# Kernel tuning notes

Measured on AMD Instinct MI355X. Metric: run time of the kernel, lower is better.

## Reference

```python
import jax, jax.numpy as jnp
import numpy as np

K = 256      # model / per-head dim (module uses full k per head)
H = 8        # heads
B = 4
T = 2048
EPS = 1e-5   # nn.LayerNorm default eps


def _layernorm(x, gamma, beta):
    mu = jnp.mean(x, axis=-1, keepdims=True)
    var = jnp.mean(jnp.square(x - mu), axis=-1, keepdims=True)
    return (x - mu) * jax.lax.rsqrt(var + EPS) * gamma + beta


def setup_inputs() -> dict:
    key = jax.random.key(0)
    ks = jax.random.split(key, 12)
    s = lambda fan_in: 1.0 / np.sqrt(fan_in)
    return {
        "x":  jax.random.normal(ks[0], (B, T, K), dtype=jnp.float32),
        # attention projections, stored (in, out) for x @ W
        "wq": jax.random.uniform(ks[1], (K, K * H), jnp.float32, -s(K), s(K)),
        "wk": jax.random.uniform(ks[2], (K, K * H), jnp.float32, -s(K), s(K)),
        "wv": jax.random.uniform(ks[3], (K, K * H), jnp.float32, -s(K), s(K)),
        "wu": jax.random.uniform(ks[4], (K * H, K), jnp.float32, -s(K * H), s(K * H)),
        "bu": jnp.zeros((K,), jnp.float32),
        # feed-forward
        "w1": jax.random.uniform(ks[5], (K, 4 * K), jnp.float32, -s(K), s(K)),
        "b1": jnp.zeros((4 * K,), jnp.float32),
        "w2": jax.random.uniform(ks[6], (4 * K, K), jnp.float32, -s(4 * K), s(4 * K)),
        "b2": jnp.zeros((K,), jnp.float32),
        # layernorms
        "g1": jnp.ones((K,), jnp.float32),
        "be1": jnp.zeros((K,), jnp.float32),
        "g2": jnp.ones((K,), jnp.float32),
        "be2": jnp.zeros((K,), jnp.float32),
    }


def reference(x, wq, wk, wv, wu, bu, w1, b1, w2, b2, g1, be1, g2, be2):
    b, t, k = x.shape
    h = H
    scale = k ** (-0.25)  # applied to both q and k, as in the torch code
    q = (x @ wq).reshape(b, t, h, k).transpose(0, 2, 1, 3) * scale  # bhtk
    kk = (x @ wk).reshape(b, t, h, k).transpose(0, 2, 1, 3) * scale
    v = (x @ wv).reshape(b, t, h, k).transpose(0, 2, 1, 3)
    dot = jnp.einsum("bhtk,bhsk->bhts", q, kk)
    # masked=True: upper triangle (offset=1) set to -inf -> causal
    causal = jnp.tril(jnp.ones((t, t), dtype=bool))
    dot = jnp.where(causal, dot, -jnp.inf)
    attn = jax.nn.softmax(dot, axis=-1)
    out = jnp.einsum("bhts,bhsk->bhtk", attn, v)
    out = out.transpose(0, 2, 1, 3).reshape(b, t, h * k)
    attn_out = out @ wu + bu

    x = x + attn_out                    # residual=True
    x = _layernorm(x, g1, be1)          # norm=True
    ff = jnp.maximum(x @ w1 + b1, 0.0) @ w2 + b2
    x = x + ff                          # ff + residual
    x = _layernorm(x, g2, be2)
    return x
```

## Files before the change

kernel.cpp:

```cpp
#include <hip/hip_runtime.h>
#include <hip/hip_bf16.h>

#define TT 2048
#define BB 4
#define HH 8
#define KK 256
#define MM (BB*TT)
#define NQKV 6144
#define QKS 4096

typedef __attribute__((ext_vector_type(8))) short bf16x8;
typedef __attribute__((ext_vector_type(4))) float f32x4;

__device__ __forceinline__ void gld_lds16(const void* g, void* lds) {
    __builtin_amdgcn_global_load_lds(
        (const __attribute__((address_space(1))) unsigned int*)g,
        (__attribute__((address_space(3))) unsigned int*)lds, 16, 0, 0);
}

__global__ __launch_bounds__(256) void cvt_k(const float* __restrict__ in,
                                             __hip_bfloat16* __restrict__ out, int n) {
    int i = (blockIdx.x * 256 + threadIdx.x) * 4;
    if (i + 3 < n) {
        float4 v = *(const float4*)(in + i);
        out[i + 0] = __float2bfloat16(v.x);
        out[i + 1] = __float2bfloat16(v.y);
        out[i + 2] = __float2bfloat16(v.z);
        out[i + 3] = __float2bfloat16(v.w);
    }
}

__global__ __launch_bounds__(256) void transpose_cvt(const float* __restrict__ in,
                                                     __hip_bfloat16* __restrict__ out,
                                                     int R, int C) {
    __shared__ float tile[32][33];
    int c0 = blockIdx.x * 32, r0 = blockIdx.y * 32;
    int tx = threadIdx.x & 31, ty = threadIdx.x >> 5;
    #pragma unroll
    for (int i = ty; i < 32; i += 8)
        tile[i][tx] = in[(size_t)(r0 + i) * C + c0 + tx];
    __syncthreads();
    #pragma unroll
    for (int i = ty; i < 32; i += 8)
        out[(size_t)(c0 + i) * R + r0 + tx] = __float2bfloat16(tile[tx][i]);
}

template<int EPI, int BN>
__global__ __launch_bounds__(256) void gemm_k(const __hip_bfloat16* __restrict__ A,
                                              const __hip_bfloat16* __restrict__ Bt,
                                              int M, int N, int Kd,
                                              const float* __restrict__ bias,
                                              const float* __restrict__ res,
                                              void* __restrict__ outp, float scale,
                                              __hip_bfloat16* __restrict__ vtp) {
    __shared__ short sA[2][128 * 32];
    __shared__ short sB[2][BN * 32];
    int tid = threadIdx.x, lane = tid & 63, wave = tid >> 6;
    int l15 = lane & 15, g = lane >> 4;
    int m0 = blockIdx.y * 128, n0 = blockIdx.x * BN;
    constexpr int NF = BN / 32;
    int wm = (wave >> 1) * 64, wn = (wave & 1) * (BN / 2);
    f32x4 acc[4][NF] = {};
    const int NT = Kd >> 5;

    int arow0 = tid >> 2, acol = (tid & 3) * 8;
    int arow1 = (tid + 256) >> 2;

    auto STAGE = [&](int kt, int buf) {
        size_t ka = (size_t)kt * 32 + acol;
        gld_lds16(A + (size_t)(m0 + arow0) * Kd + ka, (char*)sA[buf] + wave * 1024);
        gld_lds16(A + (size_t)(m0 + arow1) * Kd + ka, (char*)sA[buf] + 4096 + wave * 1024);
        gld_lds16(Bt + (size_t)(n0 + arow0) * Kd + ka, (char*)sB[buf] + wave * 1024);
        if (BN == 128)
            gld_lds16(Bt + (size_t)(n0 + arow1) * Kd + ka, (char*)sB[buf] + 4096 + wave * 1024);
    };

    STAGE(0, 0);
    asm volatile("s_waitcnt vmcnt(0)" ::: "memory");
    __syncthreads();
    int cur = 0;
    for (int kt = 0; kt < NT; ++kt) {
        if (kt + 1 < NT) STAGE(kt + 1, cur ^ 1);
        bf16x8 af[4], bfr[NF];
        #pragma unroll
        for (int mf = 0; mf < 4; ++mf)
            af[mf] = *(const bf16x8*)&sA[cur][(wm + mf * 16 + l15) * 32 + g * 8];
        #pragma unroll
        for (int nf = 0; nf < NF; ++nf)
            bfr[nf] = *(const bf16x8*)&sB[cur][(wn + nf * 16 + l15) * 32 + g * 8];
        #pragma unroll
        for (int mf = 0; mf < 4; ++mf)
            #pragma unroll
            for (int nf = 0; nf < NF; ++nf)
                acc[mf][nf] = __builtin_amdgcn_mfma_f32_16x16x32_bf16(af[mf], bfr[nf], acc[mf][nf], 0, 0, 0);
        asm volatile("s_waitcnt vmcnt(0)" ::: "memory");
        __syncthreads();
        cur ^= 1;
    }

    #pragma unroll
    for (int mf = 0; mf < 4; ++mf) {
        int rowb = m0 + wm + mf * 16 + g * 4;
        #pragma unroll
        for (int nf = 0; nf < NF; ++nf) {
            int col = n0 + wn + nf * 16 + l15;
            if (EPI == 0) {
                if (col < 4096) {
                    #pragma unroll
                    for (int r = 0; r < 4; ++r)
                        ((__hip_bfloat16*)outp)[(size_t)(rowb + r) * QKS + col] =
                            __float2bfloat16(acc[mf][nf][r] * scale);
                } else {
                    int hv = col - 4096, h = hv >> 8, d = hv & 255;
                    int b = rowb >> 11, t = rowb & 2047;
                    ushort4 w;
                    w.x = __bfloat16_as_ushort(__float2bfloat16(acc[mf][nf][0]));
                    w.y = __bfloat16_as_ushort(__float2bfloat16(acc[mf][nf][1]));
                    w.z = __bfloat16_as_ushort(__float2bfloat16(acc[mf][nf][2]));
                    w.w = __bfloat16_as_ushort(__float2bfloat16(acc[mf][nf][3]));
                    *(ushort4*)(vtp + ((size_t)((b * 8 + h) * 256 + d)) * TT + t) = w;
                }
            } else {
                #pragma unroll
                for (int r = 0; r < 4; ++r) {
                    float v = acc[mf][nf][r];
                    size_t idx = (size_t)(rowb + r) * N + col;
                    if (EPI == 1) {
                        ((float*)outp)[idx] = v + bias[col] + res[idx];
                    } else {
                        v += bias[col];
                        ((__hip_bfloat16*)outp)[idx] = __float2bfloat16(v > 0.0f ? v : 0.0f);
                    }
                }
            }
        }
    }
}

__global__ __launch_bounds__(512, 2) void attn_k(const __hip_bfloat16* __restrict__ QK,
                                                 const __hip_bfloat16* __restrict__ VT,
                                                 __hip_bfloat16* __restrict__ O) {
    __shared__ char Kl[2][32768];
    __shared__ char Vl[2][32768];
    __shared__ char Pl[8][2048];
    int tid = threadIdx.x, lane = tid & 63, wave = tid >> 6;
    int id = blockIdx.x;
    int xcd = id & 7, w = id >> 3;
    int bh = xcd * 4 + (w >> 3);
    int jtp = w & 7;
    int b = bh >> 3, h = bh & 7;
    const __hip_bfloat16* Qb = QK + (size_t)b * TT * QKS + h * KK;
    const __hip_bfloat16* Kb = Qb + 2048;
    const __hip_bfloat16* Vtb = VT + (size_t)bh * KK * TT;

    int l15 = lane & 15, g = lane >> 4;
    int koff = g * 8;
    int koffB = g * 16;
    int pswz = (l15 & 7) << 4;

    auto STAGE = [&](int s0, int buf) {
        #pragma unroll
        for (int rd = 0; rd < 4; ++rd) {
            int L = rd * 8192 + tid * 16;
            int row = L >> 9;
            int cb = (L & 511) ^ ((row & 7) << 4);
            gld_lds16((const char*)(Kb + (size_t)(s0 + row) * QKS) + cb,
                      Kl[buf] + rd * 8192 + wave * 1024);
        }
        #pragma unroll
        for (int rd = 0; rd < 4; ++rd) {
            int L = rd * 8192 + tid * 16;
            int row = L >> 7;
            int cb = (L & 127) ^ ((row & 7) << 4);
            gld_lds16((const char*)(Vtb + (size_t)row * TT + s0) + cb,
                      Vl[buf] + rd * 8192 + wave * 1024);
        }
    };

    #pragma unroll 1
    for (int half = 0; half < 2; ++half) {
        int jt = (half == 0) ? jtp : 15 - jtp;
        int q0 = jt * 128;
        int rowbase = q0 + wave * 16;
        bf16x8 qf[8];
        #pragma unroll
        for (int kk = 0; kk < 8; ++kk)
            qf[kk] = *(const bf16x8*)(Qb + (size_t)(rowbase + l15) * QKS + kk * 32 + koff);

        f32x4 Oa[16] = {};
        float mrow = -__builtin_inff();
        float lrow = 0.f;

        STAGE(0, 0);
        asm volatile("s_waitcnt vmcnt(0)" ::: "memory");
        __syncthreads();
        int cur = 0;
        const int niter = 2 * jt + 2;

        #pragma unroll 1
        for (int i = 0; i < niter; ++i) {
            int s0 = i * 64;
            if (i + 1 < niter) STAGE(s0 + 64, cur ^ 1);

            if (s0 <= rowbase + 15) {
                f32x4 S[4] = {};
                __builtin_amdgcn_s_setprio(1);
                #pragma unroll
                for (int nf = 0; nf < 4; ++nf) {
                    int r = nf * 16 + l15;
                    int swz = (r & 7) << 4;
                    #pragma unroll
                    for (int kk = 0; kk < 8; ++kk) {
                        bf16x8 kf = *(const bf16x8*)(Kl[cur] + r * 512 + ((kk * 64 + koffB) ^ swz));
                        S[nf] = __builtin_amdgcn_mfma_f32_16x16x32_bf16(kf, qf[kk], S[nf], 0, 0, 0);
                    }
                }
                __builtin_amdgcn_s_setprio(0);
                if (s0 + 63 > rowbase) {
                    int qg = rowbase + l15;
                    #pragma unroll
                    for (int nf = 0; nf < 4; ++nf)
                        #pragma unroll
                        for (int r = 0; r < 4; ++r) {
                            int sg = s0 + nf * 16 + g * 4 + r;
                            if (sg > qg) S[nf][r] = -__builtin_inff();
                        }
                }
                float mx = S[0][0];
                #pragma unroll
                for (int nf = 0; nf < 4; ++nf)
                    #pragma unroll
                    for (int r = 0; r < 4; ++r) mx = fmaxf(mx, S[nf][r]);
                mx = fmaxf(mx, __shfl_xor(mx, 16));
                mx = fmaxf(mx, __shfl_xor(mx, 32));
                if (__any(mx > mrow + 8.0f)) {
                    float mn = fmaxf(mrow, mx);
                    float alpha = exp2f(mrow - mn);
                    mrow = mn;
                    lrow *= alpha;
                    float al[4];
                    #pragma unroll
                    for (int r = 0; r < 4; ++r) al[r] = __shfl(alpha, (g << 2) + r);
                    #pragma unroll
                    for (int nf2 = 0; nf2 < 16; ++nf2)
                        #pragma unroll
                        for (int r = 0; r < 4; ++r) Oa[nf2][r] *= al[r];
                }
                float ps = 0.f;
                #pragma unroll
                for (int nf = 0; nf < 4; ++nf)
                    #pragma unroll
                    for (int r = 0; r < 4; ++r) {
                        float p = exp2f(S[nf][r] - mrow);
                        S[nf][r] = p; ps += p;
                    }
                ps += __shfl_xor(ps, 16);
                ps += __shfl_xor(ps, 32);
                lrow += ps;
                #pragma unroll
                for (int nf = 0; nf < 4; ++nf) {
                    uint2 pk2;
                    pk2.x = (unsigned)__bfloat16_as_ushort(__float2bfloat16(S[nf][0]))
                          | ((unsigned)__bfloat16_as_ushort(__float2bfloat16(S[nf][1])) << 16);
                    pk2.y = (unsigned)__bfloat16_as_ushort(__float2bfloat16(S[nf][2]))
                          | ((unsigned)__bfloat16_as_ushort(__float2bfloat16(S[nf][3])) << 16);
                    *(uint2*)(Pl[wave] + l15 * 128 + ((nf * 32 + g * 8) ^ pswz)) = pk2;
                }
                bf16x8 pa[2];
                #pragma unroll
                for (int kk2 = 0; kk2 < 2; ++kk2)
                    pa[kk2] = *(const bf16x8*)(Pl[wave] + l15 * 128 + ((kk2 * 64 + koffB) ^ pswz));
                __builtin_amdgcn_s_setprio(1);
                #pragma unroll
                for (int nf2 = 0; nf2 < 16; ++nf2) {
                    int r = nf2 * 16 + l15;
                    int swz = (r & 7) << 4;
                    #pragma unroll
                    for (int kk2 = 0; kk2 < 2; ++kk2) {
                        bf16x8 vb = *(const bf16x8*)(Vl[cur] + r * 128 + ((kk2 * 64 + koffB) ^ swz));
                        Oa[nf2] = __builtin_amdgcn_mfma_f32_16x16x32_bf16(pa[kk2], vb, Oa[nf2], 0, 0, 0);
                    }
                }
                __builtin_amdgcn_s_setprio(0);
            }
            asm volatile("s_waitcnt vmcnt(0)" ::: "memory");
            __syncthreads();
            cur ^= 1;
        }
        float rcp_ = 1.0f / lrow;
        float rc[4];
        #pragma unroll
        for (int r = 0; r < 4; ++r) rc[r] = __shfl(rcp_, (g << 2) + r);
        #pragma unroll
        for (int nf2 = 0; nf2 < 16; ++nf2) {
            int col = nf2 * 16 + l15;
            #pragma unroll
            for (int r = 0; r < 4; ++r) {
                int t = rowbase + g * 4 + r;
                O[((size_t)b * TT + t) * 2048 + h * KK + col] = __float2bfloat16(Oa[nf2][r] * rc[r]);
            }
        }
    }
}

__global__ __launch_bounds__(256) void layernorm_k(const float* __restrict__ y,
                                                   const float* __restrict__ g,
                                                   const float* __restrict__ be,
                                                   float* __restrict__ out_f,
                                                   __hip_bfloat16* __restrict__ out_b) {
    int row = blockIdx.x * 4 + (threadIdx.x >> 6);
    int lane = threadIdx.x & 63;
    float4 v = *(const float4*)(y + (size_t)row * 256 + lane * 4);
    float s = v.x + v.y + v.z + v.w;
    #pragma unroll
    for (int d = 1; d < 64; d <<= 1) s += __shfl_xor(s, d);
    float mu = s * (1.0f / 256.0f);
    float dx = v.x - mu, dy = v.y - mu, dz = v.z - mu, dw = v.w - mu;
    float q = dx * dx + dy * dy + dz * dz + dw * dw;
    #pragma unroll
    for (int d = 1; d < 64; d <<= 1) q += __shfl_xor(q, d);
    float rs = rsqrtf(q * (1.0f / 256.0f) + 1e-5f);
    float4 gg = *(const float4*)(g + lane * 4);
    float4 bb = *(const float4*)(be + lane * 4);
    float4 o;
    o.x = dx * rs * gg.x + bb.x;
    o.y = dy * rs * gg.y + bb.y;
    o.z = dz * rs * gg.z + bb.z;
    o.w = dw * rs * gg.w + bb.w;
    *(float4*)(out_f + (size_t)row * 256 + lane * 4) = o;
    if (out_b) {
        size_t i = (size_t)row * 256 + lane * 4;
        out_b[i + 0] = __float2bfloat16(o.x);
        out_b[i + 1] = __float2bfloat16(o.y);
        out_b[i + 2] = __float2bfloat16(o.z);
        out_b[i + 3] = __float2bfloat16(o.w);
    }
}

extern "C" void kernel_launch(void* const* d_in, const int* in_sizes, int n_in,
                              void* d_out, int out_size, void* d_ws, size_t ws_size,
                              hipStream_t stream) {
    const float* x  = (const float*)d_in[0];
    const float* wq = (const float*)d_in[1];
    const float* wk = (const float*)d_in[2];
    const float* wv = (const float*)d_in[3];
    const float* wu = (const float*)d_in[4];
    const float* bu = (const float*)d_in[5];
    const float* w1 = (const float*)d_in[6];
    const float* b1 = (const float*)d_in[7];
    const float* w2 = (const float*)d_in[8];
    const float* b2 = (const float*)d_in[9];
    const float* g1 = (const float*)d_in[10];
    const float* be1 = (const float*)d_in[11];
    const float* g2 = (const float*)d_in[12];
    const float* be2 = (const float*)d_in[13];

    char* p = (char*)d_ws;
    auto alloc = [&](size_t bytes) { char* r = p; p += bytes; return r; };
    __hip_bfloat16* xb    = (__hip_bfloat16*)alloc((size_t)MM * KK * 2);
    __hip_bfloat16* wqkvT = (__hip_bfloat16*)alloc((size_t)NQKV * KK * 2);
    __hip_bfloat16* wuT   = (__hip_bfloat16*)alloc((size_t)KK * 2048 * 2);
    __hip_bfloat16* w1T   = (__hip_bfloat16*)alloc((size_t)1024 * KK * 2);
    __hip_bfloat16* w2T   = (__hip_bfloat16*)alloc((size_t)KK * 1024 * 2);
    __hip_bfloat16* qk    = (__hip_bfloat16*)alloc((size_t)MM * QKS * 2);
    __hip_bfloat16* vt    = (__hip_bfloat16*)alloc((size_t)32 * KK * TT * 2);
    __hip_bfloat16* attn  = (__hip_bfloat16*)alloc((size_t)MM * 2048 * 2);
    float*          y1    = (float*)alloc((size_t)MM * KK * 4);
    float*          x1    = (float*)alloc((size_t)MM * KK * 4);
    __hip_bfloat16* x1b   = (__hip_bfloat16*)alloc((size_t)MM * KK * 2);
    __hip_bfloat16* hid   = (__hip_bfloat16*)alloc((size_t)MM * 1024 * 2);
    float*          y2    = (float*)alloc((size_t)MM * KK * 4);

    cvt_k<<<(MM * KK) / 1024, 256, 0, stream>>>(x, xb, MM * KK);
    transpose_cvt<<<dim3(64, 8),  256, 0, stream>>>(wq, wqkvT,             256, 2048);
    transpose_cvt<<<dim3(64, 8),  256, 0, stream>>>(wk, wqkvT + 2048 * 256, 256, 2048);
    transpose_cvt<<<dim3(64, 8),  256, 0, stream>>>(wv, wqkvT + 4096 * 256, 256, 2048);
    transpose_cvt<<<dim3(8, 64),  256, 0, stream>>>(wu, wuT, 2048, 256);
    transpose_cvt<<<dim3(32, 8),  256, 0, stream>>>(w1, w1T, 256, 1024);
    transpose_cvt<<<dim3(8, 32),  256, 0, stream>>>(w2, w2T, 1024, 256);

    gemm_k<0, 128><<<dim3(NQKV / 128, MM / 128), 256, 0, stream>>>(
        xb, wqkvT, MM, NQKV, 256, nullptr, nullptr, qk, 0.3002806f, vt);

    attn_k<<<dim3(256), 512, 0, stream>>>(qk, vt, attn);

    gemm_k<1, 64><<<dim3(4, MM / 128), 256, 0, stream>>>(
        attn, wuT, MM, 256, 2048, bu, x, y1, 1.0f, nullptr);
    layernorm_k<<<MM / 4, 256, 0, stream>>>(y1, g1, be1, x1, x1b);

    gemm_k<2, 128><<<dim3(8, MM / 128), 256, 0, stream>>>(
        x1b, w1T, MM, 1024, 256, b1, nullptr, hid, 1.0f, nullptr);
    gemm_k<1, 64><<<dim3(4, MM / 128), 256, 0, stream>>>(
        hid, w2T, MM, 256, 1024, b2, x1, y2, 1.0f, nullptr);
    layernorm_k<<<MM / 4, 256, 0, stream>>>(y2, g2, be2, (float*)d_out, nullptr);
}
```

Baseline: 260.3 us.

## Restructure attention to 4-wave blocks with 32 query rows per wave, single-buffered

The attention kernel moves from 512-thread blocks that each process two causal tiles to 512 blocks of 256 threads, each handling one query tile. Each wave now owns 32 query rows, so every K and V fragment read from LDS feeds two MFMAs. K/V staging drops double buffering, so loads are no longer overlapped with compute, in exchange for half the LDS per block. Separately, the GEMM LDS tiles gain an XOR swizzle on the A/B rows to reduce bank conflicts.

```diff
diff --git a/kernel.cpp b/kernel.cpp
--- a/kernel.cpp
+++ b/kernel.cpp
@@ -63,11 +63,12 @@
     f32x4 acc[4][NF] = {};
     const int NT = Kd >> 5;
 
-    int arow0 = tid >> 2, acol = (tid & 3) * 8;
-    int arow1 = (tid + 256) >> 2;
+    int arow0 = tid >> 2;
+    int arow1 = arow0 + 64;
+    int sl = ((tid & 3) ^ ((arow0 >> 1) & 3)) * 8;
 
     auto STAGE = [&](int kt, int buf) {
-        size_t ka = (size_t)kt * 32 + acol;
+        size_t ka = (size_t)kt * 32 + sl;
         gld_lds16(A + (size_t)(m0 + arow0) * Kd + ka, (char*)sA[buf] + wave * 1024);
         gld_lds16(A + (size_t)(m0 + arow1) * Kd + ka, (char*)sA[buf] + 4096 + wave * 1024);
         gld_lds16(Bt + (size_t)(n0 + arow0) * Kd + ka, (char*)sB[buf] + wave * 1024);
@@ -83,11 +84,15 @@
         if (kt + 1 < NT) STAGE(kt + 1, cur ^ 1);
         bf16x8 af[4], bfr[NF];
         #pragma unroll
-        for (int mf = 0; mf < 4; ++mf)
-            af[mf] = *(const bf16x8*)&sA[cur][(wm + mf * 16 + l15) * 32 + g * 8];
-        #pragma unroll
-        for (int nf = 0; nf < NF; ++nf)
-            bfr[nf] = *(const bf16x8*)&sB[cur][(wn + nf * 16 + l15) * 32 + g * 8];
+        for (int mf = 0; mf < 4; ++mf) {
+            int row = wm + mf * 16 + l15;
+            af[mf] = *(const bf16x8*)((char*)sA[cur] + row * 64 + ((g ^ ((row >> 1) & 3)) * 16));
+        }
+        #pragma unroll
+        for (int nf = 0; nf < NF; ++nf) {
+            int row = wn + nf * 16 + l15;
+            bfr[nf] = *(const bf16x8*)((char*)sB[cur] + row * 64 + ((g ^ ((row >> 1) & 3)) * 16));
+        }
         #pragma unroll
         for (int mf = 0; mf < 4; ++mf)
             #pragma unroll
@@ -137,17 +142,18 @@
     }
 }
 
-__global__ __launch_bounds__(512, 2) void attn_k(const __hip_bfloat16* __restrict__ QK,
+__global__ __launch_bounds__(256, 2) void attn_k(const __hip_bfloat16* __restrict__ QK,
                                                  const __hip_bfloat16* __restrict__ VT,
                                                  __hip_bfloat16* __restrict__ O) {
-    __shared__ char Kl[2][32768];
-    __shared__ char Vl[2][32768];
-    __shared__ char Pl[8][2048];
+    __shared__ char Kl[32768];
+    __shared__ char Vl[32768];
+    __shared__ char Pl[4][4096];
     int tid = threadIdx.x, lane = tid & 63, wave = tid >> 6;
     int id = blockIdx.x;
     int xcd = id & 7, w = id >> 3;
-    int bh = xcd * 4 + (w >> 3);
-    int jtp = w & 7;
+    int half = w >> 5, w5 = w & 31;
+    int bh = xcd * 4 + (w5 & 3);
+    int jt = half ? (w5 >> 2) : 15 - (w5 >> 2);
     int b = bh >> 3, h = bh & 7;
     const __hip_bfloat16* Qb = QK + (size_t)b * TT * QKS + h * KK;
     const __hip_bfloat16* Kb = Qb + 2048;
@@ -158,136 +164,142 @@
     int koffB = g * 16;
     int pswz = (l15 & 7) << 4;
 
-    auto STAGE = [&](int s0, int buf) {
-        #pragma unroll
-        for (int rd = 0; rd < 4; ++rd) {
-            int L = rd * 8192 + tid * 16;
+    auto STAGE = [&](int s0) {
+        #pragma unroll
+        for (int rd = 0; rd < 8; ++rd) {
+            int L = rd * 4096 + tid * 16;
             int row = L >> 9;
             int cb = (L & 511) ^ ((row & 7) << 4);
             gld_lds16((const char*)(Kb + (size_t)(s0 + row) * QKS) + cb,
-                      Kl[buf] + rd * 8192 + wave * 1024);
-        }
-        #pragma unroll
-        for (int rd = 0; rd < 4; ++rd) {
-            int L = rd * 8192 + tid * 16;
+                      Kl + rd * 4096 + wave * 1024);
+        }
+        #pragma unroll
+        for (int rd = 0; rd < 8; ++rd) {
+            int L = rd * 4096 + tid * 16;
             int row = L >> 7;
             int cb = (L & 127) ^ ((row & 7) << 4);
             gld_lds16((const char*)(Vtb + (size_t)row * TT + s0) + cb,
-                      Vl[buf] + rd * 8192 + wave * 1024);
+                      Vl + rd * 4096 + wave * 1024);
         }
     };
 
+    int q0 = jt * 128;
+    int rowbase = q0 + wave * 32;
+    bf16x8 qf[2][8];
+    #pragma unroll
+    for (int f = 0; f < 2; ++f)
+        #pragma unroll
+        for (int kk = 0; kk < 8; ++kk)
+            qf[f][kk] = *(const bf16x8*)(Qb + (size_t)(rowbase + f * 16 + l15) * QKS + kk * 32 + koff);
+
+    f32x4 Oa[2][16] = {};
+    float mrow[2] = {-__builtin_inff(), -__builtin_inff()};
+    float lrow[2] = {0.f, 0.f};
+    const int niter = 2 * jt + 2;
+
     #pragma unroll 1
-    for (int half = 0; half < 2; ++half) {
-        int jt = (half == 0) ? jtp : 15 - jtp;
-        int q0 = jt * 128;
-        int rowbase = q0 + wave * 16;
-        bf16x8 qf[8];
-        #pragma unroll
-        for (int kk = 0; kk < 8; ++kk)
-            qf[kk] = *(const bf16x8*)(Qb + (size_t)(rowbase + l15) * QKS + kk * 32 + koff);
-
-        f32x4 Oa[16] = {};
-        float mrow = -__builtin_inff();
-        float lrow = 0.f;
-
-        STAGE(0, 0);
+    for (int i = 0; i < niter; ++i) {
+        int s0 = i * 64;
+        STAGE(s0);
         asm volatile("s_waitcnt vmcnt(0)" ::: "memory");
         __syncthreads();
-        int cur = 0;
-        const int niter = 2 * jt + 2;
-
-        #pragma unroll 1
-        for (int i = 0; i < niter; ++i) {
-            int s0 = i * 64;
-            if (i + 1 < niter) STAGE(s0 + 64, cur ^ 1);
-
-            if (s0 <= rowbase + 15) {
-                f32x4 S[4] = {};
-                __builtin_amdgcn_s_setprio(1);
-                #pragma unroll
-                for (int nf = 0; nf < 4; ++nf) {
-                    int r = nf * 16 + l15;
-                    int swz = (r & 7) << 4;
-                    #pragma unroll
-                    for (int kk = 0; kk < 8; ++kk) {
-                        bf16x8 kf = *(const bf16x8*)(Kl[cur] + r * 512 + ((kk * 64 + koffB) ^ swz));
-                        S[nf] = __builtin_amdgcn_mfma_f32_16x16x32_bf16(kf, qf[kk], S[nf], 0, 0, 0);
-                    }
-                }
-                __builtin_amdgcn_s_setprio(0);
-                if (s0 + 63 > rowbase) {
-                    int qg = rowbase + l15;
+
+        if (s0 <= rowbase + 31) {
+            f32x4 S[2][4] = {{}, {}};
+            __builtin_amdgcn_s_setprio(1);
+            #pragma unroll
+            for (int nf = 0; nf < 4; ++nf) {
+                int r = nf * 16 + l15;
+                int swz = (r & 7) << 4;
+                #pragma unroll
+                for (int kk = 0; kk < 8; ++kk) {
+                    bf16x8 kf = *(const bf16x8*)(Kl + r * 512 + ((kk * 64 + koffB) ^ swz));
+                    S[0][nf] = __builtin_amdgcn_mfma_f32_16x16x32_bf16(kf, qf[0][kk], S[0][nf], 0, 0, 0);
+                    S[1][nf] = __builtin_amdgcn_mfma_f32_16x16x32_bf16(kf, qf[1][kk], S[1][nf], 0, 0, 0);
+                }
+            }
+            __builtin_amdgcn_s_setprio(0);
+            if (s0 + 63 > rowbase) {
+                #pragma unroll
+                for (int f = 0; f < 2; ++f) {
+                    int qg = rowbase + f * 16 + l15;
                     #pragma unroll
                     for (int nf = 0; nf < 4; ++nf)
                         #pragma unroll
                         for (int r = 0; r < 4; ++r) {
                             int sg = s0 + nf * 16 + g * 4 + r;
-                            if (sg > qg) S[nf][r] = -__builtin_inff();
+                            if (sg > qg) S[f][nf][r] = -__builtin_inff();
                         }
                 }
-                float mx = S[0][0];
+            }
+            #pragma unroll
+            for (int f = 0; f < 2; ++f) {
+                float mx = S[f][0][0];
                 #pragma unroll
                 for (int nf = 0; nf < 4; ++nf)
                     #pragma unroll
-                    for (int r = 0; r < 4; ++r) mx = fmaxf(mx, S[nf][r]);
+                    for (int r = 0; r < 4; ++r) mx = fmaxf(mx, S[f][nf][r]);
                 mx = fmaxf(mx, __shfl_xor(mx, 16));
                 mx = fmaxf(mx, __shfl_xor(mx, 32));
-                if (__any(mx > mrow + 8.0f)) {
-                    float mn = fmaxf(mrow, mx);
-                    float alpha = exp2f(mrow - mn);
-                    mrow = mn;
-                    lrow *= alpha;
+                if (__any(mx > mrow[f] + 8.0f)) {
+                    float mn = fmaxf(mrow[f], mx);
+                    float alpha = exp2f(mrow[f] - mn);
+                    mrow[f] = mn;
+                    lrow[f] *= alpha;
                     float al[4];
                     #pragma unroll
                     for (int r = 0; r < 4; ++r) al[r] = __shfl(alpha, (g << 2) + r);
                     #pragma unroll
                     for (int nf2 = 0; nf2 < 16; ++nf2)
                         #pragma unroll
-                        for (int r = 0; r < 4; ++r) Oa[nf2][r] *= al[r];
+                        for (int r = 0; r < 4; ++r) Oa[f][nf2][r] *= al[r];
                 }
                 float ps = 0.f;
                 #pragma unroll
                 for (int nf = 0; nf < 4; ++nf)
                     #pragma unroll
                     for (int r = 0; r < 4; ++r) {
-                        float p = exp2f(S[nf][r] - mrow);
-                        S[nf][r] = p; ps += p;
+                        float p = exp2f(S[f][nf][r] - mrow[f]);
+                        S[f][nf][r] = p; ps += p;
                     }
                 ps += __shfl_xor(ps, 16);
                 ps += __shfl_xor(ps, 32);
-                lrow += ps;
+                lrow[f] += ps;
                 #pragma unroll
                 for (int nf = 0; nf < 4; ++nf) {
                     uint2 pk2;
-                    pk2.x = (unsigned)__bfloat16_as_ushort(__float2bfloat16(S[nf][0]))
-                          | ((unsigned)__bfloat16_as_ushort(__float2bfloat16(S[nf][1])) << 16);
-                    pk2.y = (unsigned)__bfloat16_as_ushort(__float2bfloat16(S[nf][2]))
-                          | ((unsigned)__bfloat16_as_ushort(__float2bfloat16(S[nf][3])) << 16);
-                    *(uint2*)(Pl[wave] + l15 * 128 + ((nf * 32 + g * 8) ^ pswz)) = pk2;
-                }
-                bf16x8 pa[2];
-                #pragma unroll
-                for (int kk2 = 0; kk2 < 2; ++kk2)
-                    pa[kk2] = *(const bf16x8*)(Pl[wave] + l15 * 128 + ((kk2 * 64 + koffB) ^ pswz));
-                __builtin_amdgcn_s_setprio(1);
-                #pragma unroll
-                for (int nf2 = 0; nf2 < 16; ++nf2) {
-                    int r = nf2 * 16 + l15;
-                    int swz = (r & 7) << 4;
-                    #pragma unroll
-                    for (int kk2 = 0; kk2 < 2; ++kk2) {
-                        bf16x8 vb = *(const bf16x8*)(Vl[cur] + r * 128 + ((kk2 * 64 + koffB) ^ swz));
-                        Oa[nf2] = __builtin_amdgcn_mfma_f32_16x16x32_bf16(pa[kk2], vb, Oa[nf2], 0, 0, 0);
-                    }
-                }
-                __builtin_amdgcn_s_setprio(0);
-            }
-            asm volatile("s_waitcnt vmcnt(0)" ::: "memory");
-            __syncthreads();
-            cur ^= 1;
-        }
-        float rcp_ = 1.0f / lrow;
+                    pk2.x = (unsigned)__bfloat16_as_ushort(__float2bfloat16(S[f][nf][0]))
+                          | ((unsigned)__bfloat16_as_ushort(__float2bfloat16(S[f][nf][1])) << 16);
+                    pk2.y = (unsigned)__bfloat16_as_ushort(__float2bfloat16(S[f][nf][2]))
+                          | ((unsigned)__bfloat16_as_ushort(__float2bfloat16(S[f][nf][3])) << 16);
+                    *(uint2*)(Pl[wave] + (f * 16 + l15) * 128 + ((nf * 32 + g * 8) ^ pswz)) = pk2;
+                }
+            }
+            bf16x8 pa0[2], pa1[2];
+            #pragma unroll
+            for (int kk2 = 0; kk2 < 2; ++kk2) {
+                pa0[kk2] = *(const bf16x8*)(Pl[wave] + (l15) * 128 + ((kk2 * 64 + koffB) ^ pswz));
+                pa1[kk2] = *(const bf16x8*)(Pl[wave] + (16 + l15) * 128 + ((kk2 * 64 + koffB) ^ pswz));
+            }
+            __builtin_amdgcn_s_setprio(1);
+            #pragma unroll
+            for (int nf2 = 0; nf2 < 16; ++nf2) {
+                int r = nf2 * 16 + l15;
+                int swz = (r & 7) << 4;
+                #pragma unroll
+                for (int kk2 = 0; kk2 < 2; ++kk2) {
+                    bf16x8 vb = *(const bf16x8*)(Vl + r * 128 + ((kk2 * 64 + koffB) ^ swz));
+                    Oa[0][nf2] = __builtin_amdgcn_mfma_f32_16x16x32_bf16(pa0[kk2], vb, Oa[0][nf2], 0, 0, 0);
+                    Oa[1][nf2] = __builtin_amdgcn_mfma_f32_16x16x32_bf16(pa1[kk2], vb, Oa[1][nf2], 0, 0, 0);
+                }
+            }
+            __builtin_amdgcn_s_setprio(0);
+        }
+        __syncthreads();
+    }
+    #pragma unroll
+    for (int f = 0; f < 2; ++f) {
+        float rcp_ = 1.0f / lrow[f];
         float rc[4];
         #pragma unroll
         for (int r = 0; r < 4; ++r) rc[r] = __shfl(rcp_, (g << 2) + r);
@@ -296,8 +308,8 @@
             int col = nf2 * 16 + l15;
             #pragma unroll
             for (int r = 0; r < 4; ++r) {
-                int t = rowbase + g * 4 + r;
-                O[((size_t)b * TT + t) * 2048 + h * KK + col] = __float2bfloat16(Oa[nf2][r] * rc[r]);
+                int t = rowbase + f * 16 + g * 4 + r;
+                O[((size_t)b * TT + t) * 2048 + h * KK + col] = __float2bfloat16(Oa[f][nf2][r] * rc[r]);
             }
         }
     }
@@ -382,7 +394,7 @@
     gemm_k<0, 128><<<dim3(NQKV / 128, MM / 128), 256, 0, stream>>>(
         xb, wqkvT, MM, NQKV, 256, nullptr, nullptr, qk, 0.3002806f, vt);
 
-    attn_k<<<dim3(256), 512, 0, stream>>>(qk, vt, attn);
+    attn_k<<<dim3(512), 256, 0, stream>>>(qk, vt, attn);
 
     gemm_k<1, 64><<<dim3(4, MM / 128), 256, 0, stream>>>(
         attn, wuT, MM, 256, 2048, bu, x, y1, 1.0f, nullptr);
```

Measured after the change: 411.1 us. 57.9% more time.

## Widen GEMM K-tile to 64 with XOR-swizzled LDS layout

Applied to the files above, without the earlier changes.

The GEMM main loop now stages 64-wide K slices per iteration instead of 32, halving the number of barrier and wait round-trips, and performs two MFMA sub-steps per stage. LDS rows are laid out with an XOR swizzle so the 16-byte fragment reads avoid bank conflicts. This doubles shared memory use per block, which may lower occupancy, and relies on Kd being a multiple of 64.

```diff
diff --git a/kernel.cpp b/kernel.cpp
--- a/kernel.cpp
+++ b/kernel.cpp
@@ -53,26 +53,36 @@
                                               const float* __restrict__ res,
                                               void* __restrict__ outp, float scale,
                                               __hip_bfloat16* __restrict__ vtp) {
-    __shared__ short sA[2][128 * 32];
-    __shared__ short sB[2][BN * 32];
+    constexpr int NF = BN / 32;
+    constexpr int BPHYS = BN / 4;
+    __shared__ short sA[2][128 * 64];
+    __shared__ short sB[2][BN * 64];
     int tid = threadIdx.x, lane = tid & 63, wave = tid >> 6;
     int l15 = lane & 15, g = lane >> 4;
     int m0 = blockIdx.y * 128, n0 = blockIdx.x * BN;
-    constexpr int NF = BN / 32;
     int wm = (wave >> 1) * 64, wn = (wave & 1) * (BN / 2);
     f32x4 acc[4][NF] = {};
-    const int NT = Kd >> 5;
-
-    int arow0 = tid >> 2, acol = (tid & 3) * 8;
-    int arow1 = (tid + 256) >> 2;
+    const int NT = Kd >> 6;
 
     auto STAGE = [&](int kt, int buf) {
-        size_t ka = (size_t)kt * 32 + acol;
-        gld_lds16(A + (size_t)(m0 + arow0) * Kd + ka, (char*)sA[buf] + wave * 1024);
-        gld_lds16(A + (size_t)(m0 + arow1) * Kd + ka, (char*)sA[buf] + 4096 + wave * 1024);
-        gld_lds16(Bt + (size_t)(n0 + arow0) * Kd + ka, (char*)sB[buf] + wave * 1024);
-        if (BN == 128)
-            gld_lds16(Bt + (size_t)(n0 + arow1) * Kd + ka, (char*)sB[buf] + 4096 + wave * 1024);
+        #pragma unroll
+        for (int c = 0; c < 4; ++c) {
+            int L = c * 4096 + tid * 16;
+            int phys = L >> 9;
+            int vp = ((L >> 4) & 31) ^ phys;
+            int row = (vp >> 3) * 32 + phys;
+            gld_lds16(A + (size_t)(m0 + row) * Kd + kt * 64 + (vp & 7) * 8,
+                      (char*)sA[buf] + L);
+        }
+        #pragma unroll
+        for (int c = 0; c < BN / 32; ++c) {
+            int L = c * 4096 + tid * 16;
+            int phys = L >> 9;
+            int vp = ((L >> 4) & 31) ^ phys;
+            int row = (vp >> 3) * BPHYS + phys;
+            gld_lds16(Bt + (size_t)(n0 + row) * Kd + kt * 64 + (vp & 7) * 8,
+                      (char*)sB[buf] + L);
+        }
     };
 
     STAGE(0, 0);
@@ -81,18 +91,27 @@
     int cur = 0;
     for (int kt = 0; kt < NT; ++kt) {
         if (kt + 1 < NT) STAGE(kt + 1, cur ^ 1);
-        bf16x8 af[4], bfr[NF];
-        #pragma unroll
-        for (int mf = 0; mf < 4; ++mf)
-            af[mf] = *(const bf16x8*)&sA[cur][(wm + mf * 16 + l15) * 32 + g * 8];
-        #pragma unroll
-        for (int nf = 0; nf < NF; ++nf)
-            bfr[nf] = *(const bf16x8*)&sB[cur][(wn + nf * 16 + l15) * 32 + g * 8];
-        #pragma unroll
-        for (int mf = 0; mf < 4; ++mf)
+        #pragma unroll
+        for (int kk = 0; kk < 2; ++kk) {
+            bf16x8 af[4], bfr[NF];
             #pragma unroll
-            for (int nf = 0; nf < NF; ++nf)
-                acc[mf][nf] = __builtin_amdgcn_mfma_f32_16x16x32_bf16(af[mf], bfr[nf], acc[mf][nf], 0, 0, 0);
+            for (int mf = 0; mf < 4; ++mf) {
+                int R = wm + mf * 16 + l15;
+                int v = (((R >> 5) << 3) + (kk << 2) + g) ^ (R & 31);
+                af[mf] = *(const bf16x8*)((char*)sA[cur] + ((R & 31) << 9) + (v << 4));
+            }
+            #pragma unroll
+            for (int nf = 0; nf < NF; ++nf) {
+                int R = wn + nf * 16 + l15;
+                int v = ((R / BPHYS) * 8 + (kk << 2) + g) ^ (R & (BPHYS - 1));
+                bfr[nf] = *(const bf16x8*)((char*)sB[cur] + ((R & (BPHYS - 1)) << 9) + (v << 4));
+            }
+            #pragma unroll
+            for (int mf = 0; mf < 4; ++mf)
+                #pragma unroll
+                for (int nf = 0; nf < NF; ++nf)
+                    acc[mf][nf] = __builtin_amdgcn_mfma_f32_16x16x32_bf16(af[mf], bfr[nf], acc[mf][nf], 0, 0, 0);
+        }
         asm volatile("s_waitcnt vmcnt(0)" ::: "memory");
         __syncthreads();
         cur ^= 1;
```

After: 259.1 us. About the same (-0.5%).
